# Performance work log

Measured on AMD Instinct MI355X. Metric: run time of the kernel, lower is better.

The kernel has to match this reference:

```python
import jax, jax.numpy as jnp
import numpy as np

RADIUS = 5
KS = 2 * RADIUS + 1  # 11
SIGMA_X2 = 4.0 ** 2  # 16
SIGMA_I2 = 10.0 ** 2  # 100


def _patches(x):
    """x: [N,1,H,W] -> [N, H*W, KS, KS] zero-padded sliding windows (torch Unfold semantics)."""
    N, _, H, W = x.shape
    p = jax.lax.conv_general_dilated_patches(
        x, (KS, KS), (1, 1), [(RADIUS, RADIUS), (RADIUS, RADIUS)]
    )  # [N, KS*KS, H, W], channel dim ordered (kh, kw)
    return p.reshape(N, KS, KS, H * W).transpose(0, 3, 1, 2)


def _distance_map(dtype):
    d = (jnp.arange(KS, dtype=dtype) - RADIUS) ** 2
    return jnp.exp(-(d[:, None] + d[None, :]) / SIGMA_X2)  # [KS, KS]


def setup_inputs() -> dict:
    key = jax.random.key(0)
    k1, k2 = jax.random.split(key)
    images = jax.random.uniform(k1, (8, 1, 224, 224), dtype=jnp.float32)
    labels = jax.random.uniform(k2, (8, 4, 224, 224), dtype=jnp.float32)
    return {"images": images, "labels": labels}


def reference(images, labels):
    B, _, H, W = images.shape
    K = labels.shape[1]
    HW = H * W

    img = images * 255.0
    regions = _patches(img)                                   # [B,HW,KS,KS]
    mask = _patches(jnp.ones((1, 1, H, W), img.dtype))        # [1,HW,KS,KS], 0 on padding
    dist_map = _distance_map(img.dtype)                       # [KS,KS]

    i_f = img.reshape(B, HW)[:, :, None, None]                # center pixel intensity
    weights = dist_map * jnp.exp(-(regions - i_f) ** 2 / SIGMA_I2) * mask  # [B,HW,KS,KS]

    # class-prob patches for all classes at once
    P = _patches(labels.reshape(B * K, 1, H, W)).reshape(B, K, HW, KS, KS)

    num = jnp.einsum('bnij,bknij->bkn', weights, P)           # sum_j w_ij * p_j
    den = weights.sum(axis=(2, 3))                            # [B,HW], sum_j w_ij
    p_f = labels.reshape(B, K, HW)

    ratio = jnp.einsum('bkn,bkn->bk', p_f, num) / jnp.einsum('bkn,bn->bk', p_f, den)
    # per-class L1Loss(ratio, 0) = mean over batch of |ratio|; summed over classes
    ratio_sum = jnp.abs(ratio).mean(axis=0).sum()
    return K - ratio_sum
```

## Files before the change

### kernel.cpp

```cpp
#include <hip/hip_runtime.h>
#include <hip/hip_bf16.h>

typedef float f2 __attribute__((ext_vector_type(2)));
typedef float f4 __attribute__((ext_vector_type(4)));

constexpr int Hh = 224, Ww = 224, Bb = 8, Kc = 4, RAD = 5;

constexpr int TX = 32;
constexpr int TILEH = 16;
constexpr int SW = TX + 2 * RAD;
constexpr int SH = TILEH + 2 * RAD;
constexpr int SSTR = SW + 1;
constexpr int GXD = Ww / TX;
constexpr int GYD = Hh / TILEH;
constexpr int PB = GXD * GYD;

constexpr float LOG2E = 1.44269504f;
constexpr float KI = -0.01f * LOG2E;
constexpr float DSC = -0.0625f * LOG2E;
constexpr float D2[12] = {25.f,16.f,9.f,4.f,1.f,0.f,1.f,4.f,9.f,16.f,25.f,0.f};

static __device__ inline f4 splat4(float x) { return (f4){x, x, x, x}; }

__global__ __launch_bounds__(256, 3) void ncut_main(const float* __restrict__ images,
                                                    const float* __restrict__ labels,
                                                    float* __restrict__ acc) {
    __shared__ float simg[SH * SSTR];
    __shared__ f4    slab[SH * SSTR];
    __shared__ float red[4][8];

    const int b   = blockIdx.z;
    const int x0  = blockIdx.x * TX;
    const int y0  = blockIdx.y * TILEH;
    const int tid = threadIdx.x;

    const float* imgb = images + (size_t)b * (Hh * Ww);
    const float* labb = labels + (size_t)b * (Kc * Hh * Ww);

    for (int idx = tid; idx < SH * SSTR; idx += 256) {
        const int lx = idx % SSTR, ly = idx / SSTR;
        const int gx = x0 - RAD + lx, gy = y0 - RAD + ly;
        float iv = 1e19f;
        f4 lv = (f4){0.f, 0.f, 0.f, 0.f};
        if (lx < SW && gx >= 0 && gx < Ww && gy >= 0 && gy < Hh) {
            const int g = gy * Ww + gx;
            iv = imgb[g] * 255.0f;
            lv = (f4){labb[g], labb[Hh * Ww + g], labb[2 * Hh * Ww + g], labb[3 * Hh * Ww + g]};
        }
        simg[idx] = iv;
        slab[idx] = lv;
    }
    __syncthreads();

    const int tx = tid & 31;
    const int ty = tid >> 5;
    const int r0 = 2 * ty;

    const float c0 = simg[(r0 + RAD) * SSTR + tx + RAD];
    const float c1 = simg[(r0 + RAD + 1) * SSTR + tx + RAD];

    f4 num0 = splat4(0.f), num1 = splat4(0.f);
    f2 den0 = (f2){0.f, 0.f}, den1 = (f2){0.f, 0.f};

#pragma unroll
    for (int dr = 0; dr < 12; ++dr) {
        const int rowoff = (r0 + dr) * SSTR + tx;
#pragma unroll
        for (int i = 0; i < 6; ++i) {
            const f2 v  = (f2){simg[rowoff + 2 * i], simg[rowoff + 2 * i + 1]};
            const f4 p0 = slab[rowoff + 2 * i];
            const f4 p1 = slab[rowoff + 2 * i + 1];
            if (dr < 11) {
                const f2 base = (f2){(D2[2 * i] + D2[dr]) * DSC,
                                     (D2[2 * i + 1] + D2[dr]) * DSC};
                const f2 d = v - c0;
                const f2 a = __builtin_elementwise_fma(d * KI, d, base);
                const float e0 = __builtin_amdgcn_exp2f(a.x);
                const float e1 = __builtin_amdgcn_exp2f(a.y);
                den0 += (f2){e0, e1};
                num0 = __builtin_elementwise_fma(splat4(e0), p0, num0);
                num0 = __builtin_elementwise_fma(splat4(e1), p1, num0);
            }
            if (dr >= 1) {
                const f2 base = (f2){(D2[2 * i] + D2[dr - 1]) * DSC,
                                     (D2[2 * i + 1] + D2[dr - 1]) * DSC};
                const f2 d = v - c1;
                const f2 a = __builtin_elementwise_fma(d * KI, d, base);
                const float e0 = __builtin_amdgcn_exp2f(a.x);
                const float e1 = __builtin_amdgcn_exp2f(a.y);
                den1 += (f2){e0, e1};
                num1 = __builtin_elementwise_fma(splat4(e0), p0, num1);
                num1 = __builtin_elementwise_fma(splat4(e1), p1, num1);
            }
        }
    }

    const f4 pc0 = slab[(r0 + RAD) * SSTR + tx + RAD];
    const f4 pc1 = slab[(r0 + RAD + 1) * SSTR + tx + RAD];
    const float dn0 = den0.x + den0.y;
    const float dn1 = den1.x + den1.y;

    const f4 numv = pc0 * num0 + pc1 * num1;
    const f4 denv = pc0 * dn0 + pc1 * dn1;

    float vals[8] = {numv.x, numv.y, numv.z, numv.w, denv.x, denv.y, denv.z, denv.w};

#pragma unroll
    for (int i = 0; i < 8; ++i) {
        float v = vals[i];
#pragma unroll
        for (int off = 32; off > 0; off >>= 1) v += __shfl_down(v, off, 64);
        vals[i] = v;
    }

    const int wave = tid >> 6, lane = tid & 63;
    if (lane == 0) {
#pragma unroll
        for (int i = 0; i < 8; ++i) red[wave][i] = vals[i];
    }
    __syncthreads();

    if (tid < 8) {
        const int gid = blockIdx.x + GXD * blockIdx.y + GXD * GYD * blockIdx.z;
        acc[gid * 8 + tid] = red[0][tid] + red[1][tid] + red[2][tid] + red[3][tid];
    }
}

__global__ void ncut_final(const float* __restrict__ acc, float* __restrict__ out) {
    const int t = threadIdx.x;
    const int k = t & 3, b = (t >> 2) & 7, part = t >> 5;
    float s = 0.f;
    for (int j = 0; j < PB; ++j) s += acc[(b * PB + j) * 8 + k + 4 * part];
    const float den = __shfl(s, (t + 32) & 63, 64);
    float r = (t < 32) ? fabsf(s / den) : 0.f;
#pragma unroll
    for (int off = 32; off > 0; off >>= 1) r += __shfl_down(r, off, 64);
    if (t == 0) out[0] = (float)Kc - r * (1.0f / (float)Bb);
}

extern "C" void kernel_launch(void* const* d_in, const int* in_sizes, int n_in,
                              void* d_out, int out_size, void* d_ws, size_t ws_size,
                              hipStream_t stream) {
    const float* images = (const float*)d_in[0];
    const float* labels = (const float*)d_in[1];
    float* out = (float*)d_out;
    float* acc = (float*)d_ws;

    dim3 grid(GXD, GYD, Bb);
    ncut_main<<<grid, 256, 0, stream>>>(images, labels, acc);
    ncut_final<<<1, 64, 0, stream>>>(acc, out);
}
```

Measured before the change: 84.04 us.

## Compute four output rows per thread, store labels as fp16 in LDS

Each thread now handles four vertically adjacent pixels instead of two, so every loaded image/label neighbor row is reused across four centers, and the block shrinks to 128 threads. The exponent is re-expanded algebraically (precomputed -2K·c and K·c² terms plus per-row beta), which removes a subtraction per tap. Labels are stored as half precision in shared memory to halve LDS footprint and bandwidth, at some precision cost. The final reduction kernel also spreads its loop over 256 threads. The outer row loop is no longer unrolled, and the expanded exponent form may lose accuracy for large intensity differences.

Measured after the change: 113.6 us. 1.35x slower.

```diff
diff --git a/kernel.cpp b/kernel.cpp
--- a/kernel.cpp
+++ b/kernel.cpp
@@ -1,13 +1,15 @@
 #include <hip/hip_runtime.h>
-#include <hip/hip_bf16.h>
 
 typedef float f2 __attribute__((ext_vector_type(2)));
 typedef float f4 __attribute__((ext_vector_type(4)));
+typedef _Float16 h4 __attribute__((ext_vector_type(4)));
 
 constexpr int Hh = 224, Ww = 224, Bb = 8, Kc = 4, RAD = 5;
 
 constexpr int TX = 32;
 constexpr int TILEH = 16;
+constexpr int PPT = 4;
+constexpr int NTHR = TX * (TILEH / PPT);
 constexpr int SW = TX + 2 * RAD;
 constexpr int SH = TILEH + 2 * RAD;
 constexpr int SSTR = SW + 1;
@@ -18,16 +20,17 @@
 constexpr float LOG2E = 1.44269504f;
 constexpr float KI = -0.01f * LOG2E;
 constexpr float DSC = -0.0625f * LOG2E;
-constexpr float D2[12] = {25.f,16.f,9.f,4.f,1.f,0.f,1.f,4.f,9.f,16.f,25.f,0.f};
+constexpr float DC[12] = {25.f * DSC, 16.f * DSC, 9.f * DSC, 4.f * DSC, 1.f * DSC, 0.f,
+                          1.f * DSC, 4.f * DSC, 9.f * DSC, 16.f * DSC, 25.f * DSC, -1e5f};
 
 static __device__ inline f4 splat4(float x) { return (f4){x, x, x, x}; }
 
-__global__ __launch_bounds__(256, 3) void ncut_main(const float* __restrict__ images,
-                                                    const float* __restrict__ labels,
-                                                    float* __restrict__ acc) {
+__global__ __launch_bounds__(NTHR, 4) void ncut_main(const float* __restrict__ images,
+                                                     const float* __restrict__ labels,
+                                                     float* __restrict__ acc) {
     __shared__ float simg[SH * SSTR];
-    __shared__ f4    slab[SH * SSTR];
-    __shared__ float red[4][8];
+    __shared__ h4    slab[SH * SSTR];
+    __shared__ float red[2][8];
 
     const int b   = blockIdx.z;
     const int x0  = blockIdx.x * TX;
@@ -37,80 +40,104 @@
     const float* imgb = images + (size_t)b * (Hh * Ww);
     const float* labb = labels + (size_t)b * (Kc * Hh * Ww);
 
-    for (int idx = tid; idx < SH * SSTR; idx += 256) {
+    for (int idx = tid; idx < SH * SSTR; idx += NTHR) {
         const int lx = idx % SSTR, ly = idx / SSTR;
         const int gx = x0 - RAD + lx, gy = y0 - RAD + ly;
         float iv = 1e19f;
-        f4 lv = (f4){0.f, 0.f, 0.f, 0.f};
+        h4 lv = (h4){(_Float16)0.f, (_Float16)0.f, (_Float16)0.f, (_Float16)0.f};
         if (lx < SW && gx >= 0 && gx < Ww && gy >= 0 && gy < Hh) {
             const int g = gy * Ww + gx;
             iv = imgb[g] * 255.0f;
-            lv = (f4){labb[g], labb[Hh * Ww + g], labb[2 * Hh * Ww + g], labb[3 * Hh * Ww + g]};
+            lv = (h4){(_Float16)labb[g], (_Float16)labb[Hh * Ww + g],
+                      (_Float16)labb[2 * Hh * Ww + g], (_Float16)labb[3 * Hh * Ww + g]};
         }
         simg[idx] = iv;
         slab[idx] = lv;
     }
     __syncthreads();
 
-    const int tx = tid & 31;
+    const int tx = tid & (TX - 1);
     const int ty = tid >> 5;
-    const int r0 = 2 * ty;
+    const int r0 = PPT * ty;
 
-    const float c0 = simg[(r0 + RAD) * SSTR + tx + RAD];
-    const float c1 = simg[(r0 + RAD + 1) * SSTR + tx + RAD];
+    float q1[PPT], kc2[PPT];
+#pragma unroll
+    for (int p = 0; p < PPT; ++p) {
+        const float c = simg[(r0 + p + RAD) * SSTR + tx + RAD];
+        q1[p]  = (-2.0f * KI) * c;
+        kc2[p] = (KI * c) * c;
+    }
 
-    f4 num0 = splat4(0.f), num1 = splat4(0.f);
-    f2 den0 = (f2){0.f, 0.f}, den1 = (f2){0.f, 0.f};
+    f4 num[PPT];
+    f2 den[PPT];
+#pragma unroll
+    for (int p = 0; p < PPT; ++p) {
+        num[p] = (f4){0.f, 0.f, 0.f, 0.f};
+        den[p] = (f2){0.f, 0.f};
+    }
+
+    const f2 kis = (f2){KI, KI};
+
+#pragma unroll 1
+    for (int dr = 0; dr < 11 + PPT - 1; ++dr) {
+        const int rowoff = (r0 + dr) * SSTR + tx;
+
+        float beta[PPT];
+#pragma unroll
+        for (int p = 0; p < PPT; ++p) {
+            const float fdy = (float)(dr - p - RAD);
+            beta[p] = __builtin_fmaf(DSC * fdy, fdy, kc2[p]);
+        }
 
 #pragma unroll
-    for (int dr = 0; dr < 12; ++dr) {
-        const int rowoff = (r0 + dr) * SSTR + tx;
+        for (int h = 0; h < 2; ++h) {
+            const int bi = 3 * h;
+            f2 v[3];
+            f4 a0[3], a1[3];
 #pragma unroll
-        for (int i = 0; i < 6; ++i) {
-            const f2 v  = (f2){simg[rowoff + 2 * i], simg[rowoff + 2 * i + 1]};
-            const f4 p0 = slab[rowoff + 2 * i];
-            const f4 p1 = slab[rowoff + 2 * i + 1];
-            if (dr < 11) {
-                const f2 base = (f2){(D2[2 * i] + D2[dr]) * DSC,
-                                     (D2[2 * i + 1] + D2[dr]) * DSC};
-                const f2 d = v - c0;
-                const f2 a = __builtin_elementwise_fma(d * KI, d, base);
-                const float e0 = __builtin_amdgcn_exp2f(a.x);
-                const float e1 = __builtin_amdgcn_exp2f(a.y);
-                den0 += (f2){e0, e1};
-                num0 = __builtin_elementwise_fma(splat4(e0), p0, num0);
-                num0 = __builtin_elementwise_fma(splat4(e1), p1, num0);
+            for (int i = 0; i < 3; ++i) {
+                const int off = rowoff + 2 * (bi + i);
+                v[i]  = (f2){simg[off], simg[off + 1]};
+                a0[i] = __builtin_convertvector(slab[off], f4);
+                a1[i] = __builtin_convertvector(slab[off + 1], f4);
             }
-            if (dr >= 1) {
-                const f2 base = (f2){(D2[2 * i] + D2[dr - 1]) * DSC,
-                                     (D2[2 * i + 1] + D2[dr - 1]) * DSC};
-                const f2 d = v - c1;
-                const f2 a = __builtin_elementwise_fma(d * KI, d, base);
-                const float e0 = __builtin_amdgcn_exp2f(a.x);
-                const float e1 = __builtin_amdgcn_exp2f(a.y);
-                den1 += (f2){e0, e1};
-                num1 = __builtin_elementwise_fma(splat4(e0), p0, num1);
-                num1 = __builtin_elementwise_fma(splat4(e1), p1, num1);
+#pragma unroll
+            for (int p = 0; p < PPT; ++p) {
+                if (dr >= p && dr <= p + 10) {
+#pragma unroll
+                    for (int i = 0; i < 3; ++i) {
+                        const int col = bi + i;
+                        const f2 dc = (f2){DC[2 * col], DC[2 * col + 1]};
+                        const f2 t1 = __builtin_elementwise_fma(v[i], kis, (f2){q1[p], q1[p]});
+                        const f2 t2 = __builtin_elementwise_fma(v[i], t1, dc);
+                        const float e0 = __builtin_amdgcn_exp2f(t2.x + beta[p]);
+                        const float e1 = __builtin_amdgcn_exp2f(t2.y + beta[p]);
+                        den[p] += (f2){e0, e1};
+                        num[p] = __builtin_elementwise_fma(splat4(e0), a0[i], num[p]);
+                        num[p] = __builtin_elementwise_fma(splat4(e1), a1[i], num[p]);
+                    }
+                }
             }
         }
     }
 
-    const f4 pc0 = slab[(r0 + RAD) * SSTR + tx + RAD];
-    const f4 pc1 = slab[(r0 + RAD + 1) * SSTR + tx + RAD];
-    const float dn0 = den0.x + den0.y;
-    const float dn1 = den1.x + den1.y;
-
-    const f4 numv = pc0 * num0 + pc1 * num1;
-    const f4 denv = pc0 * dn0 + pc1 * dn1;
+    f4 numv = splat4(0.f), denv = splat4(0.f);
+#pragma unroll
+    for (int p = 0; p < PPT; ++p) {
+        const f4 pc = __builtin_convertvector(slab[(r0 + p + RAD) * SSTR + tx + RAD], f4);
+        const float dn = den[p].x + den[p].y;
+        numv = __builtin_elementwise_fma(pc, num[p], numv);
+        denv = __builtin_elementwise_fma(pc, splat4(dn), denv);
+    }
 
     float vals[8] = {numv.x, numv.y, numv.z, numv.w, denv.x, denv.y, denv.z, denv.w};
 
 #pragma unroll
     for (int i = 0; i < 8; ++i) {
-        float v = vals[i];
+        float vv = vals[i];
 #pragma unroll
-        for (int off = 32; off > 0; off >>= 1) v += __shfl_down(v, off, 64);
-        vals[i] = v;
+        for (int off = 32; off > 0; off >>= 1) vv += __shfl_down(vv, off, 64);
+        vals[i] = vv;
     }
 
     const int wave = tid >> 6, lane = tid & 63;
@@ -122,20 +149,30 @@
 
     if (tid < 8) {
         const int gid = blockIdx.x + GXD * blockIdx.y + GXD * GYD * blockIdx.z;
-        acc[gid * 8 + tid] = red[0][tid] + red[1][tid] + red[2][tid] + red[3][tid];
+        acc[gid * 8 + tid] = red[0][tid] + red[1][tid];
     }
 }
 
 __global__ void ncut_final(const float* __restrict__ acc, float* __restrict__ out) {
+    __shared__ float red[4][64];
     const int t = threadIdx.x;
-    const int k = t & 3, b = (t >> 2) & 7, part = t >> 5;
+    const int combo = t & 63;
+    const int chunk = t >> 6;
+    const int k = combo & 3, b = (combo >> 2) & 7;
+    const int part = combo >> 5;
     float s = 0.f;
-    for (int j = 0; j < PB; ++j) s += acc[(b * PB + j) * 8 + k + 4 * part];
-    const float den = __shfl(s, (t + 32) & 63, 64);
-    float r = (t < 32) ? fabsf(s / den) : 0.f;
+    for (int j = chunk; j < PB; j += 4)
+        s += acc[(b * PB + j) * 8 + k + 4 * part];
+    red[chunk][combo] = s;
+    __syncthreads();
+    if (t < 64) {
+        float v = red[0][t] + red[1][t] + red[2][t] + red[3][t];
+        const float den = __shfl(v, (t + 32) & 63, 64);
+        float r = (t < 32) ? fabsf(v / den) : 0.f;
 #pragma unroll
-    for (int off = 32; off > 0; off >>= 1) r += __shfl_down(r, off, 64);
-    if (t == 0) out[0] = (float)Kc - r * (1.0f / (float)Bb);
+        for (int off = 32; off > 0; off >>= 1) r += __shfl_down(r, off, 64);
+        if (t == 0) out[0] = (float)Kc - r * (1.0f / (float)Bb);
+    }
 }
 
 extern "C" void kernel_launch(void* const* d_in, const int* in_sizes, int n_in,
@@ -147,6 +184,6 @@
     float* acc = (float*)d_ws;
 
     dim3 grid(GXD, GYD, Bb);
-    ncut_main<<<grid, 256, 0, stream>>>(images, labels, acc);
-    ncut_final<<<1, 64, 0, stream>>>(acc, out);
+    ncut_main<<<grid, NTHR, 0, stream>>>(images, labels, acc);
+    ncut_final<<<1, 256, 0, stream>>>(acc, out);
 }
```

## Halve tile height, store labels as fp16, expand exponent quadratic

Applied to the files above, without the earlier changes.

Halves the tile height so each block has 128 threads and twice as many blocks exist, storing label slabs in LDS as fp16 to cut shared memory footprint and bandwidth. The intensity-weight exponent is rewritten as a precomputed quadratic in the neighbor value, removing a subtraction per weight. The final reduction is spread over 256 threads. The trade-offs are larger relative halo loading overhead, fp16 conversion cost and reduced label precision.

New measurement: 102.9 us. 22.4% more time.

```diff
diff --git a/kernel.cpp b/kernel.cpp
--- a/kernel.cpp
+++ b/kernel.cpp
@@ -1,13 +1,15 @@
 #include <hip/hip_runtime.h>
-#include <hip/hip_bf16.h>
 
 typedef float f2 __attribute__((ext_vector_type(2)));
 typedef float f4 __attribute__((ext_vector_type(4)));
+typedef _Float16 h4 __attribute__((ext_vector_type(4)));
 
 constexpr int Hh = 224, Ww = 224, Bb = 8, Kc = 4, RAD = 5;
 
 constexpr int TX = 32;
-constexpr int TILEH = 16;
+constexpr int TILEH = 8;
+constexpr int PPT = 2;
+constexpr int NTHR = TX * (TILEH / PPT);
 constexpr int SW = TX + 2 * RAD;
 constexpr int SH = TILEH + 2 * RAD;
 constexpr int SSTR = SW + 1;
@@ -18,16 +20,17 @@
 constexpr float LOG2E = 1.44269504f;
 constexpr float KI = -0.01f * LOG2E;
 constexpr float DSC = -0.0625f * LOG2E;
-constexpr float D2[12] = {25.f,16.f,9.f,4.f,1.f,0.f,1.f,4.f,9.f,16.f,25.f,0.f};
+constexpr float DC[12] = {25.f * DSC, 16.f * DSC, 9.f * DSC, 4.f * DSC, 1.f * DSC, 0.f,
+                          1.f * DSC, 4.f * DSC, 9.f * DSC, 16.f * DSC, 25.f * DSC, -1e5f};
 
 static __device__ inline f4 splat4(float x) { return (f4){x, x, x, x}; }
 
-__global__ __launch_bounds__(256, 3) void ncut_main(const float* __restrict__ images,
-                                                    const float* __restrict__ labels,
-                                                    float* __restrict__ acc) {
+__global__ __launch_bounds__(NTHR, 4) void ncut_main(const float* __restrict__ images,
+                                                     const float* __restrict__ labels,
+                                                     float* __restrict__ acc) {
     __shared__ float simg[SH * SSTR];
-    __shared__ f4    slab[SH * SSTR];
-    __shared__ float red[4][8];
+    __shared__ h4    slab[SH * SSTR];
+    __shared__ float red[2][8];
 
     const int b   = blockIdx.z;
     const int x0  = blockIdx.x * TX;
@@ -37,57 +40,69 @@
     const float* imgb = images + (size_t)b * (Hh * Ww);
     const float* labb = labels + (size_t)b * (Kc * Hh * Ww);
 
-    for (int idx = tid; idx < SH * SSTR; idx += 256) {
+    for (int idx = tid; idx < SH * SSTR; idx += NTHR) {
         const int lx = idx % SSTR, ly = idx / SSTR;
         const int gx = x0 - RAD + lx, gy = y0 - RAD + ly;
         float iv = 1e19f;
-        f4 lv = (f4){0.f, 0.f, 0.f, 0.f};
+        h4 lv = (h4){(_Float16)0.f, (_Float16)0.f, (_Float16)0.f, (_Float16)0.f};
         if (lx < SW && gx >= 0 && gx < Ww && gy >= 0 && gy < Hh) {
             const int g = gy * Ww + gx;
             iv = imgb[g] * 255.0f;
-            lv = (f4){labb[g], labb[Hh * Ww + g], labb[2 * Hh * Ww + g], labb[3 * Hh * Ww + g]};
+            lv = (h4){(_Float16)labb[g], (_Float16)labb[Hh * Ww + g],
+                      (_Float16)labb[2 * Hh * Ww + g], (_Float16)labb[3 * Hh * Ww + g]};
         }
         simg[idx] = iv;
         slab[idx] = lv;
     }
     __syncthreads();
 
-    const int tx = tid & 31;
+    const int tx = tid & (TX - 1);
     const int ty = tid >> 5;
-    const int r0 = 2 * ty;
+    const int r0 = PPT * ty;
 
     const float c0 = simg[(r0 + RAD) * SSTR + tx + RAD];
     const float c1 = simg[(r0 + RAD + 1) * SSTR + tx + RAD];
 
+    const float q10  = (-2.0f * KI) * c0;
+    const float q11  = (-2.0f * KI) * c1;
+    const float kc20 = (KI * c0) * c0;
+    const float kc21 = (KI * c1) * c1;
+
     f4 num0 = splat4(0.f), num1 = splat4(0.f);
     f2 den0 = (f2){0.f, 0.f}, den1 = (f2){0.f, 0.f};
+
+    const f2 kis = (f2){KI, KI};
 
 #pragma unroll
     for (int dr = 0; dr < 12; ++dr) {
         const int rowoff = (r0 + dr) * SSTR + tx;
+
+        const float dy0 = (float)((dr - 5) * (dr - 5));
+        const float dy1 = (float)((dr - 6) * (dr - 6));
+        const float beta0 = __builtin_fmaf(DSC, dy0, kc20);
+        const float beta1 = __builtin_fmaf(DSC, dy1, kc21);
+
 #pragma unroll
         for (int i = 0; i < 6; ++i) {
-            const f2 v  = (f2){simg[rowoff + 2 * i], simg[rowoff + 2 * i + 1]};
-            const f4 p0 = slab[rowoff + 2 * i];
-            const f4 p1 = slab[rowoff + 2 * i + 1];
+            const int off = rowoff + 2 * i;
+            const f2 v  = (f2){simg[off], simg[off + 1]};
+            const f4 p0 = __builtin_convertvector(slab[off], f4);
+            const f4 p1 = __builtin_convertvector(slab[off + 1], f4);
+            const f2 dc = (f2){DC[2 * i], DC[2 * i + 1]};
             if (dr < 11) {
-                const f2 base = (f2){(D2[2 * i] + D2[dr]) * DSC,
-                                     (D2[2 * i + 1] + D2[dr]) * DSC};
-                const f2 d = v - c0;
-                const f2 a = __builtin_elementwise_fma(d * KI, d, base);
-                const float e0 = __builtin_amdgcn_exp2f(a.x);
-                const float e1 = __builtin_amdgcn_exp2f(a.y);
+                const f2 t1 = __builtin_elementwise_fma(v, kis, (f2){q10, q10});
+                const f2 t2 = __builtin_elementwise_fma(v, t1, dc + (f2){beta0, beta0});
+                const float e0 = __builtin_amdgcn_exp2f(t2.x);
+                const float e1 = __builtin_amdgcn_exp2f(t2.y);
                 den0 += (f2){e0, e1};
                 num0 = __builtin_elementwise_fma(splat4(e0), p0, num0);
                 num0 = __builtin_elementwise_fma(splat4(e1), p1, num0);
             }
             if (dr >= 1) {
-                const f2 base = (f2){(D2[2 * i] + D2[dr - 1]) * DSC,
-                                     (D2[2 * i + 1] + D2[dr - 1]) * DSC};
-                const f2 d = v - c1;
-                const f2 a = __builtin_elementwise_fma(d * KI, d, base);
-                const float e0 = __builtin_amdgcn_exp2f(a.x);
-                const float e1 = __builtin_amdgcn_exp2f(a.y);
+                const f2 t1 = __builtin_elementwise_fma(v, kis, (f2){q11, q11});
+                const f2 t2 = __builtin_elementwise_fma(v, t1, dc + (f2){beta1, beta1});
+                const float e0 = __builtin_amdgcn_exp2f(t2.x);
+                const float e1 = __builtin_amdgcn_exp2f(t2.y);
                 den1 += (f2){e0, e1};
                 num1 = __builtin_elementwise_fma(splat4(e0), p0, num1);
                 num1 = __builtin_elementwise_fma(splat4(e1), p1, num1);
@@ -95,8 +110,8 @@
         }
     }
 
-    const f4 pc0 = slab[(r0 + RAD) * SSTR + tx + RAD];
-    const f4 pc1 = slab[(r0 + RAD + 1) * SSTR + tx + RAD];
+    const f4 pc0 = __builtin_convertvector(slab[(r0 + RAD) * SSTR + tx + RAD], f4);
+    const f4 pc1 = __builtin_convertvector(slab[(r0 + RAD + 1) * SSTR + tx + RAD], f4);
     const float dn0 = den0.x + den0.y;
     const float dn1 = den1.x + den1.y;
 
@@ -107,10 +122,10 @@
 
 #pragma unroll
     for (int i = 0; i < 8; ++i) {
-        float v = vals[i];
+        float vv = vals[i];
 #pragma unroll
-        for (int off = 32; off > 0; off >>= 1) v += __shfl_down(v, off, 64);
-        vals[i] = v;
+        for (int off = 32; off > 0; off >>= 1) vv += __shfl_down(vv, off, 64);
+        vals[i] = vv;
     }
 
     const int wave = tid >> 6, lane = tid & 63;
@@ -122,20 +137,30 @@
 
     if (tid < 8) {
         const int gid = blockIdx.x + GXD * blockIdx.y + GXD * GYD * blockIdx.z;
-        acc[gid * 8 + tid] = red[0][tid] + red[1][tid] + red[2][tid] + red[3][tid];
+        acc[gid * 8 + tid] = red[0][tid] + red[1][tid];
     }
 }
 
 __global__ void ncut_final(const float* __restrict__ acc, float* __restrict__ out) {
+    __shared__ float red[4][64];
     const int t = threadIdx.x;
-    const int k = t & 3, b = (t >> 2) & 7, part = t >> 5;
+    const int combo = t & 63;
+    const int chunk = t >> 6;
+    const int k = combo & 3, b = (combo >> 2) & 7;
+    const int part = combo >> 5;
     float s = 0.f;
-    for (int j = 0; j < PB; ++j) s += acc[(b * PB + j) * 8 + k + 4 * part];
-    const float den = __shfl(s, (t + 32) & 63, 64);
-    float r = (t < 32) ? fabsf(s / den) : 0.f;
+    for (int j = chunk; j < PB; j += 4)
+        s += acc[(b * PB + j) * 8 + k + 4 * part];
+    red[chunk][combo] = s;
+    __syncthreads();
+    if (t < 64) {
+        float v = red[0][t] + red[1][t] + red[2][t] + red[3][t];
+        const float den = __shfl(v, (t + 32) & 63, 64);
+        float r = (t < 32) ? fabsf(v / den) : 0.f;
 #pragma unroll
-    for (int off = 32; off > 0; off >>= 1) r += __shfl_down(r, off, 64);
-    if (t == 0) out[0] = (float)Kc - r * (1.0f / (float)Bb);
+        for (int off = 32; off > 0; off >>= 1) r += __shfl_down(r, off, 64);
+        if (t == 0) out[0] = (float)Kc - r * (1.0f / (float)Bb);
+    }
 }
 
 extern "C" void kernel_launch(void* const* d_in, const int* in_sizes, int n_in,
@@ -147,6 +172,6 @@
     float* acc = (float*)d_ws;
 
     dim3 grid(GXD, GYD, Bb);
-    ncut_main<<<grid, 256, 0, stream>>>(images, labels, acc);
-    ncut_final<<<1, 64, 0, stream>>>(acc, out);
+    ncut_main<<<grid, NTHR, 0, stream>>>(images, labels, acc);
+    ncut_final<<<1, 256, 0, stream>>>(acc, out);
 }
```
